# Performance work log

Hardware: AMD Instinct MI355X
Metric: run time of the kernel (lower is better)

The kernel has to match this reference:

```python
import jax, jax.numpy as jnp
import numpy as np

# dims: batch, seq, model dim, heads, head_k_dim, head_v_dim, conv size
B, S, D, H, DK, DV, K = 1, 2048, 1024, 8, 128, 128, 4
KD, VD = H * DK, H * DV  # key_dim, value_dim


def _silu(x):
    return x * jax.nn.sigmoid(x)


def _l2norm(x, eps=1e-6):
    return x * jax.lax.rsqrt(jnp.sum(x * x, -1, keepdims=True) + eps)


def _causal_conv_silu(x, w):
    # depthwise causal conv1d (ShortConvolution, activation='silu', no bias)
    # x: [b, s, d], w: [d, K]
    Kc = w.shape[1]
    xp = jnp.pad(x, ((0, 0), (Kc - 1, 0), (0, 0)))
    y = sum(xp[:, i:i + x.shape[1], :] * w[:, i] for i in range(Kc))
    return _silu(y)


def _rmsnorm(x, w, eps=1e-5):
    return x * jax.lax.rsqrt(jnp.mean(x * x, -1, keepdims=True) + eps) * w


def _kda(q, k, v, g, beta):
    # gated delta-rule linear attention (KDA), recurrent form == chunk_kda math
    # q,k,g: [B,S,H,DK]; v: [B,S,H,DV]; beta: [B,S,H]
    scale = DK ** -0.5
    qn = _l2norm(q) * scale  # use_qk_l2norm_in_kernel=True
    kn = _l2norm(k)

    def step(Sm, inp):
        q_t, k_t, v_t, g_t, b_t = inp  # [B,H,DK], [B,H,DK], [B,H,DV], [B,H,DK], [B,H]
        Sm = Sm * jnp.exp(g_t)[..., None]                    # per-key-channel decay
        v_new = (v_t - jnp.einsum('bhk,bhkv->bhv', k_t, Sm)) * b_t[..., None]
        Sm = Sm + k_t[..., None] * v_new[..., None, :]       # delta-rule update
        o_t = jnp.einsum('bhk,bhkv->bhv', q_t, Sm)
        return Sm, o_t

    xs = (jnp.swapaxes(qn, 0, 1), jnp.swapaxes(kn, 0, 1), jnp.swapaxes(v, 0, 1),
          jnp.swapaxes(g, 0, 1), jnp.swapaxes(beta, 0, 1))
    S0 = jnp.zeros((q.shape[0], H, DK, DV), jnp.float32)
    _, o = jax.lax.scan(step, S0, xs)
    return jnp.swapaxes(o, 0, 1)  # [B,S,H,DV]


def setup_inputs() -> dict:
    key = jax.random.key(0)
    ks = jax.random.split(key, 20)

    def w(k, shape, fan_in):
        return jax.random.normal(k, shape, jnp.float32) / np.sqrt(fan_in)

    return {
        'x': jax.random.normal(ks[0], (B, S, D), jnp.float32),
        've': jax.random.normal(ks[1], (B, S, D), jnp.float32),
        'sa_lambdas': jax.random.uniform(ks[2], (2,), jnp.float32),
        'Wq': w(ks[3], (KD, D), D), 'Wk': w(ks[4], (KD, D), D), 'Wv': w(ks[5], (VD, D), D),
        'Wo': w(ks[6], (D, VD), VD),
        'wq_conv': w(ks[7], (KD, K), K), 'wk_conv': w(ks[8], (KD, K), K), 'wv_conv': w(ks[9], (VD, K), K),
        'Wf1': w(ks[10], (DV, D), D), 'Wf2': w(ks[11], (KD, DV), DV),
        'Wb': w(ks[12], (H, D), D),
        'A_log': jnp.log(jax.random.uniform(ks[13], (H,), jnp.float32, 1.0, 16.0)),
        'dt_bias': jnp.zeros((KD,), jnp.float32),
        'Wg1': w(ks[14], (DV, D), D), 'Wg2': w(ks[15], (VD, DV), DV),
        'bg2': jnp.zeros((VD,), jnp.float32),
        'w_norm': jnp.ones((DV,), jnp.float32),
    }


def reference(x, ve, sa_lambdas, Wq, Wk, Wv, Wo, wq_conv, wk_conv, wv_conv,
              Wf1, Wf2, Wb, A_log, dt_bias, Wg1, Wg2, bg2, w_norm):
    b, s, _ = x.shape
    # q/k/v projections + short causal conv with silu
    q = _causal_conv_silu(x @ Wq.T, wq_conv)
    k = _causal_conv_silu(x @ Wk.T, wk_conv)
    v = _causal_conv_silu(x @ Wv.T, wv_conv)
    # fused_kda_gate: g = -exp(A_log) * softplus(f_proj(x) + dt_bias), per [H, DK]
    g = (x @ Wf1.T) @ Wf2.T
    g = jax.nn.softplus((g + dt_bias).astype(jnp.float32)).reshape(b, s, H, DK)
    g = -jnp.exp(A_log)[None, None, :, None] * g
    beta = jax.nn.sigmoid((x @ Wb.T).astype(jnp.float32))  # [b,s,H]
    q = q.reshape(b, s, H, DK)
    k = k.reshape(b, s, H, DK)
    v = v.reshape(b, s, H, DV)
    # mix v with value-embedding ve (3-D branch of _mix_v_with_ve)
    ve_v = _causal_conv_silu(ve @ Wv.T, wv_conv).reshape(b, s, H, DV)
    v = sa_lambdas[0] * v + sa_lambdas[1] * ve_v
    o = _kda(q, k, v, g, beta)  # [b,s,H,DV]
    # FusedRMSNormGated(activation='sigmoid'): rmsnorm(o)*w then gate
    g_out = ((x @ Wg1.T) @ Wg2.T + bg2).reshape(b, s, H, DV)
    o = _rmsnorm(o, w_norm) * jax.nn.sigmoid(g_out)
    return o.reshape(b, s, VD) @ Wo.T
```

## Files before the change

### kernel.cpp

```cpp
#include <hip/hip_runtime.h>
#include <math.h>
#include <stdint.h>

#define S_LEN 2048
#define DMODEL 1024
#define NH 8
#define DK_ 128
#define DV_ 128
#define KD_ 1024
#define KCONV 4
#define CW 32
#define NW2 64
#define PREB_STRIDE 17408
#define TKH_OFF 0
#define QHT_OFF 4096
#define KCT_OFF 8192
#define TV_OFF 12288
#define NN_OFF 16384
#define RS 164
#define GS 20

typedef short bf16x8 __attribute__((ext_vector_type(8)));
typedef float f32x4 __attribute__((ext_vector_type(4)));

__device__ __forceinline__ uint16_t f2bf(float f) {
  uint32_t u = __float_as_uint(f);
  u += 0x7FFF + ((u >> 16) & 1);
  return (uint16_t)(u >> 16);
}
__device__ __forceinline__ float bf2f(uint16_t u) {
  return __uint_as_float((uint32_t)u << 16);
}
__device__ __forceinline__ void glds16(const uint16_t* g, uint16_t* l) {
  __builtin_amdgcn_global_load_lds(
      (const __attribute__((address_space(1))) void*)g,
      (__attribute__((address_space(3))) void*)l, 16, 0, 0);
}
__device__ __forceinline__ float dot4(float4 a, float4 b) {
  return fmaf(a.w, b.w, fmaf(a.z, b.z, fmaf(a.y, b.y, a.x * b.x)));
}
__device__ __forceinline__ float4 f4add(float4 a, float4 b) {
  float4 r; r.x = a.x + b.x; r.y = a.y + b.y; r.z = a.z + b.z; r.w = a.w + b.w; return r;
}
__device__ __forceinline__ float4 f4sub(float4 a, float4 b) {
  float4 r; r.x = a.x - b.x; r.y = a.y - b.y; r.z = a.z - b.z; r.w = a.w - b.w; return r;
}
__device__ __forceinline__ float4 f4mul(float4 a, float4 b) {
  float4 r; r.x = a.x * b.x; r.y = a.y * b.y; r.z = a.z * b.z; r.w = a.w * b.w; return r;
}
__device__ __forceinline__ float4 f4s(float4 a, float s) {
  float4 r; r.x = a.x * s; r.y = a.y * s; r.z = a.z * s; r.w = a.w * s; return r;
}
__device__ __forceinline__ float4 f4expc(float4 a) {
  float4 r;
  r.x = expf(fminf(a.x, 0.f)); r.y = expf(fminf(a.y, 0.f));
  r.z = expf(fminf(a.z, 0.f)); r.w = expf(fminf(a.w, 0.f));
  return r;
}
__device__ __forceinline__ float4 f4exp(float4 a) {
  float4 r; r.x = expf(a.x); r.y = expf(a.y); r.z = expf(a.z); r.w = expf(a.w); return r;
}
__device__ __forceinline__ uint4 pack8(float4 a, float4 b) {
  uint4 r;
  r.x = (uint32_t)f2bf(a.x) | ((uint32_t)f2bf(a.y) << 16);
  r.y = (uint32_t)f2bf(a.z) | ((uint32_t)f2bf(a.w) << 16);
  r.z = (uint32_t)f2bf(b.x) | ((uint32_t)f2bf(b.y) << 16);
  r.w = (uint32_t)f2bf(b.z) | ((uint32_t)f2bf(b.w) << 16);
  return r;
}
__device__ __forceinline__ uint2 pack4(f32x4 a) {
  uint2 r;
  r.x = (uint32_t)f2bf(a[0]) | ((uint32_t)f2bf(a[1]) << 16);
  r.y = (uint32_t)f2bf(a[2]) | ((uint32_t)f2bf(a[3]) << 16);
  return r;
}
union U4B8 { uint4 u; bf16x8 b; };
__device__ __forceinline__ bf16x8 u2b(uint4 u) { U4B8 x; x.u = u; return x.b; }

#define DPPADD(x, ctrl) \
  x += __int_as_float(__builtin_amdgcn_update_dpp(0, __float_as_int(x), ctrl, 0xF, 0xF, true))

__device__ __forceinline__ void row8_sum2(float& a, float& b) {
  DPPADD(a, 0xB1); DPPADD(b, 0xB1);
  DPPADD(a, 0x4E); DPPADD(b, 0x4E);
  DPPADD(a, 0x141); DPPADD(b, 0x141);
}
__device__ __forceinline__ void row8_arr8x2(float* x, float* y) {
#pragma unroll
  for (int i = 0; i < 8; i++) { DPPADD(x[i], 0xB1); DPPADD(y[i], 0xB1); }
#pragma unroll
  for (int i = 0; i < 8; i++) { DPPADD(x[i], 0x4E); DPPADD(y[i], 0x4E); }
#pragma unroll
  for (int i = 0; i < 8; i++) { DPPADD(x[i], 0x141); DPPADD(y[i], 0x141); }
}

struct CastArgs {
  const float* s[8];
  uint16_t* d[8];
  int n[8];
};
__global__ __launch_bounds__(256) void cast_multi(CastArgs a) {
  int i = blockIdx.y;
  const int step = gridDim.x * 256 * 8;
  for (int base = (blockIdx.x * 256 + threadIdx.x) * 8; base < a.n[i]; base += step) {
    const float4* sp = (const float4*)(a.s[i] + base);
    float4 x0 = sp[0], x1 = sp[1];
    *(uint4*)(a.d[i] + base) = pack8(x0, x1);
  }
}

__global__ __launch_bounds__(256) void gemm_wc(
    const float* __restrict__ A,
    const float* __restrict__ B,
    uint16_t* __restrict__ C) {
  __shared__ float As[16][68];
  __shared__ float Bs[16][68];
  const int tid = threadIdx.x;
  const int m0 = blockIdx.y * 64, n0 = blockIdx.x * 64;
  const int tx = tid & 15, ty = tid >> 4;
  const int lk = tid & 15, lr = tid >> 4;
  const int bc = tid & 63, bkr = tid >> 6;
  float acc[4][4] = {};
  for (int k0 = 0; k0 < 128; k0 += 16) {
#pragma unroll
    for (int i = 0; i < 4; i++) {
      As[lk][lr + 16 * i] = A[(size_t)(m0 + lr + 16 * i) * 128 + k0 + lk];
      Bs[bkr + 4 * i][bc] = B[(size_t)(k0 + bkr + 4 * i) * 1024 + n0 + bc];
    }
    __syncthreads();
#pragma unroll
    for (int kk = 0; kk < 16; kk++) {
      float4 a4 = *(const float4*)&As[kk][ty * 4];
      float4 b4 = *(const float4*)&Bs[kk][tx * 4];
      float av[4] = {a4.x, a4.y, a4.z, a4.w};
      float bv[4] = {b4.x, b4.y, b4.z, b4.w};
#pragma unroll
      for (int i = 0; i < 4; i++)
#pragma unroll
        for (int jx = 0; jx < 4; jx++) acc[i][jx] = fmaf(av[i], bv[jx], acc[i][jx]);
    }
    __syncthreads();
  }
#pragma unroll
  for (int i = 0; i < 4; i++)
#pragma unroll
    for (int jx = 0; jx < 4; jx++)
      C[(size_t)(m0 + ty * 4 + i) * 1024 + n0 + tx * 4 + jx] = f2bf(acc[i][jx]);
}

__global__ __launch_bounds__(256) void pad_wb(const float* __restrict__ Wb,
                                              uint16_t* __restrict__ Wbp) {
  int idx = blockIdx.x * 256 + threadIdx.x;
  if (idx >= 128 * 1024) return;
  int r = idx >> 10;
  Wbp[idx] = (r < 8) ? f2bf(Wb[idx]) : (uint16_t)0;
}

struct GJobs {
  const uint16_t* A[8];
  const uint16_t* B[8];
  void* C[8];
  int N[8];
  int outbf[8];
};
__global__ __launch_bounds__(256) void gemm_mfma(GJobs j, int K) {
  const int z = blockIdx.z;
  const int N = j.N[z];
  const int n0 = blockIdx.x * 128;
  if (n0 >= N) return;
  __shared__ uint16_t Asb[128 * 32];
  __shared__ uint16_t Bsb[128 * 32];
  const uint16_t* __restrict__ A = j.A[z];
  const uint16_t* __restrict__ B = j.B[z];
  const int tid = threadIdx.x;
  const int w = tid >> 6, lane = tid & 63;
  const int m0 = blockIdx.y * 128;
  const int mw = (w & 1) * 64, nw = (w >> 1) * 64;
  const int c0 = tid, c1 = 256 + tid;
  const int r0 = c0 >> 2, cl0 = (c0 & 3) ^ ((r0 >> 2) & 3);
  const int r1 = c1 >> 2, cl1 = (c1 & 3) ^ ((r1 >> 2) & 3);
  const uint16_t* gA0 = A + (size_t)(m0 + r0) * K + cl0 * 8;
  const uint16_t* gA1 = A + (size_t)(m0 + r1) * K + cl1 * 8;
  const uint16_t* gB0 = B + (size_t)(n0 + r0) * K + cl0 * 8;
  const uint16_t* gB1 = B + (size_t)(n0 + r1) * K + cl1 * 8;
  uint16_t* lA0 = Asb + w * 512;
  uint16_t* lA1 = Asb + 2048 + w * 512;
  uint16_t* lB0 = Bsb + w * 512;
  uint16_t* lB1 = Bsb + 2048 + w * 512;

  const int l15 = lane & 15, q = lane >> 4;
  const int ccq = q ^ ((l15 >> 2) & 3);

  f32x4 acc[4][4] = {};
  for (int k0 = 0; k0 < K; k0 += 32) {
    glds16(gA0 + k0, lA0);
    glds16(gA1 + k0, lA1);
    glds16(gB0 + k0, lB0);
    glds16(gB1 + k0, lB1);
    __syncthreads();
    bf16x8 af[4], bfr[4];
#pragma unroll
    for (int i = 0; i < 4; i++)
      af[i] = *(const bf16x8*)&Asb[(mw + i * 16 + l15) * 32 + ccq * 8];
#pragma unroll
    for (int jx = 0; jx < 4; jx++)
      bfr[jx] = *(const bf16x8*)&Bsb[(nw + jx * 16 + l15) * 32 + ccq * 8];
#pragma unroll
    for (int i = 0; i < 4; i++)
#pragma unroll
      for (int jx = 0; jx < 4; jx++)
        acc[i][jx] = __builtin_amdgcn_mfma_f32_16x16x32_bf16(af[i], bfr[jx],
                                                             acc[i][jx], 0, 0, 0);
    __syncthreads();
  }
  const int obf = j.outbf[z];
#pragma unroll
  for (int i = 0; i < 4; i++) {
#pragma unroll
    for (int jx = 0; jx < 4; jx++) {
      int n = n0 + nw + jx * 16 + l15;
#pragma unroll
      for (int r = 0; r < 4; r++) {
        int m = m0 + mw + i * 16 + q * 4 + r;
        if (obf)
          ((uint16_t*)j.C[z])[(size_t)m * N + n] = f2bf(acc[i][jx][r]);
        else
          ((float*)j.C[z])[(size_t)m * N + n] = acc[i][jx][r];
      }
    }
  }
}

__global__ __launch_bounds__(256) void conv_silu_mix(
    const uint16_t* __restrict__ qp, const uint16_t* __restrict__ kp,
    const uint16_t* __restrict__ vp, const uint16_t* __restrict__ vep,
    const float* __restrict__ wq, const float* __restrict__ wk,
    const float* __restrict__ wv, const float* __restrict__ lam,
    float* __restrict__ qc, float* __restrict__ kc, float* __restrict__ vmx) {
  int idx = blockIdx.x * 256 + threadIdx.x;
  if (idx >= S_LEN * KD_) return;
  int s = idx >> 10, d = idx & 1023;
  float aq = 0.f, ak = 0.f, av = 0.f, ae = 0.f;
#pragma unroll
  for (int i = 0; i < KCONV; i++) {
    int ss = s - (KCONV - 1) + i;
    if (ss < 0) continue;
    size_t off = (size_t)ss * KD_ + d;
    aq = fmaf(bf2f(qp[off]), wq[d * KCONV + i], aq);
    ak = fmaf(bf2f(kp[off]), wk[d * KCONV + i], ak);
    av = fmaf(bf2f(vp[off]), wv[d * KCONV + i], av);
    ae = fmaf(bf2f(vep[off]), wv[d * KCONV + i], ae);
  }
  qc[idx] = aq / (1.f + expf(-aq));
  kc[idx] = ak / (1.f + expf(-ak));
  float sv = av / (1.f + expf(-av));
  float se = ae / (1.f + expf(-ae));
  vmx[idx] = lam[0] * sv + lam[1] * se;
}

__global__ __launch_bounds__(256) void kda_pre(
    const float* __restrict__ qc, const float* __restrict__ kc,
    const float* __restrict__ graw, const float* __restrict__ vm,
    const float* __restrict__ bpre, const float* __restrict__ dt_bias,
    const float* __restrict__ A_log, uint16_t* __restrict__ preB,
    float* __restrict__ preF) {
  __shared__ float kls[32 * RS];
  __shared__ float Gls[32 * RS];
  __shared__ float khls[32 * 132];
  __shared__ float Mcm[32 * 36];
  __shared__ float bls[32];
  const int w = blockIdx.x >> 3, h = blockIdx.x & 7;
  const int tid = threadIdx.x;
  const int t = tid >> 3, kq = tid & 7;
  const int wv = tid >> 6;
  const size_t gb = (size_t)blockIdx.x * PREB_STRIDE;
  const size_t gf = (size_t)blockIdx.x * 128;

  size_t roff = (size_t)(w * CW + t) * KD_ + h * DK_ + kq * 16;
  float4 kv[4], qv[4], gv[4], dtb[4];
#pragma unroll
  for (int i = 0; i < 4; i++) {
    kv[i] = *(const float4*)(kc + roff + i * 4);
    qv[i] = *(const float4*)(qc + roff + i * 4);
    gv[i] = *(const float4*)(graw + roff + i * 4);
    dtb[i] = *(const float4*)(dt_bias + h * DK_ + kq * 16 + i * 4);
  }
  const float Ahead = expf(A_log[h]);
  if (tid < 32) {
    float b = bpre[(size_t)(w * CW + tid) * 128 + h];
    bls[tid] = 1.f / (1.f + expf(-b));
  }
  float src[32];
  if (tid >= 128) {
    int c2 = tid - 128;
#pragma unroll
    for (int t2 = 0; t2 < 32; t2++)
      src[t2] = vm[(size_t)(w * CW + t2) * KD_ + h * DV_ + c2];
  }
#pragma unroll
  for (int i = 0; i < 4; i++) {
    float vsp[4];
    float xin[4] = {gv[i].x + dtb[i].x, gv[i].y + dtb[i].y,
                    gv[i].z + dtb[i].z, gv[i].w + dtb[i].w};
#pragma unroll
    for (int e = 0; e < 4; e++)
      vsp[e] = (xin[e] > 20.f) ? xin[e] : log1pf(expf(xin[e]));
    gv[i].x = -Ahead * vsp[0]; gv[i].y = -Ahead * vsp[1];
    gv[i].z = -Ahead * vsp[2]; gv[i].w = -Ahead * vsp[3];
  }
  float sk = 0.f, sq = 0.f;
#pragma unroll
  for (int i = 0; i < 4; i++) {
    sk += dot4(kv[i], kv[i]);
    sq += dot4(qv[i], qv[i]);
  }
  row8_sum2(sk, sq);
  float rkn = rsqrtf(sk + 1e-6f);
  float rqn = rsqrtf(sq + 1e-6f) * 0.08838834764831845f;
#pragma unroll
  for (int i = 0; i < 4; i++) {
    kv[i] = f4s(kv[i], rkn);
    qv[i] = f4s(qv[i], rqn);
    *(float4*)&kls[t * RS + kq * GS + i * 4] = kv[i];
    *(float4*)&Gls[t * RS + kq * GS + i * 4] = gv[i];
  }
  __syncthreads();
  float4 Ga[4] = {};
#pragma unroll
  for (int jb = 0; jb < 4; jb++) {
    if (jb <= wv) {
#pragma unroll
      for (int jj = 0; jj < 8; jj++) {
        int j = jb * 8 + jj;
        bool inc = (jb < wv) || (j <= t);
#pragma unroll
        for (int i = 0; i < 4; i++) {
          float4 gj = *(const float4*)&Gls[j * RS + kq * GS + i * 4];
          if (inc) Ga[i] = f4add(Ga[i], gj);
        }
      }
    }
  }
  __syncthreads();
  float4 Pa[4];
#pragma unroll
  for (int i = 0; i < 4; i++) {
    *(float4*)&Gls[t * RS + kq * GS + i * 4] = Ga[i];
    Pa[i] = f4exp(Ga[i]);
    float4 kh = f4mul(kv[i], Pa[i]);
    *(float4*)&khls[t * 132 + kq * 16 + i * 4] = kh;
  }
  {
    float4 q0 = f4mul(qv[0], Pa[0]), q1 = f4mul(qv[1], Pa[1]);
    float4 q2 = f4mul(qv[2], Pa[2]), q3 = f4mul(qv[3], Pa[3]);
    *(uint4*)(preB + gb + QHT_OFF + t * 128 + kq * 16) = pack8(q0, q1);
    *(uint4*)(preB + gb + QHT_OFF + t * 128 + kq * 16 + 8) = pack8(q2, q3);
  }
  if (t == 31) {
#pragma unroll
    for (int i = 0; i < 4; i++)
      *(float4*)(preF + gf + kq * 16 + i * 4) = Pa[i];
  }
  __syncthreads();
#pragma unroll
  for (int i = 0; i < 4; i++) {
    float4 Gfi = *(const float4*)&Gls[31 * RS + kq * GS + i * 4];
    float4 ea = f4expc(f4sub(Gfi, Ga[i]));
    float4 kc4 = f4mul(kv[i], ea);
    float kk[4] = {kc4.x, kc4.y, kc4.z, kc4.w};
#pragma unroll
    for (int e = 0; e < 4; e++)
      preB[gb + KCT_OFF + (kq * 16 + i * 4 + e) * 32 + t] = f2bf(kk[e]);
  }
#pragma unroll
  for (int jb = 0; jb < 4; jb++) {
    if (jb <= wv) {
      float mp8[8], np8[8];
#pragma unroll
      for (int jj = 0; jj < 8; jj++) {
        int j = jb * 8 + jj;
        float m = 0.f, n = 0.f;
#pragma unroll
        for (int i = 0; i < 4; i++) {
          float4 kj = *(const float4*)&kls[j * RS + kq * GS + i * 4];
          float4 Gj = *(const float4*)&Gls[j * RS + kq * GS + i * 4];
          float4 e = f4expc(f4sub(Ga[i], Gj));
          float4 p = f4mul(kj, e);
          m += dot4(kv[i], p);
          n += dot4(qv[i], p);
        }
        mp8[jj] = (j < t) ? m : 0.f;
        np8[jj] = (j <= t) ? n : 0.f;
      }
      row8_arr8x2(mp8, np8);
#pragma unroll
      for (int jj = 0; jj < 8; jj++) {
        if (kq == jj) {
          int j = jb * 8 + jj;
          Mcm[j * 36 + t] = bls[t] * mp8[jj];
          preB[gb + NN_OFF + t * 32 + j] = f2bf(np8[jj]);
        }
      }
    } else {
      preB[gb + NN_OFF + t * 32 + jb * 8 + kq] = 0;
    }
  }
  float bl[32];
#pragma unroll
  for (int i = 0; i < 8; i++) {
    float4 b4 = *(const float4*)&bls[i * 4];
    bl[i * 4 + 0] = b4.x; bl[i * 4 + 1] = b4.y;
    bl[i * 4 + 2] = b4.z; bl[i * 4 + 3] = b4.w;
  }
  if (tid < 128) {
#pragma unroll
    for (int t2 = 0; t2 < 32; t2++) src[t2] = khls[t2 * 132 + tid];
  }
  __syncthreads();
  const int c = tid;
  float acc[32];
#pragma unroll
  for (int i = 0; i < 32; i++) acc[i] = 0.f;
#pragma unroll
  for (int t2 = 0; t2 < 32; t2++) {
    float val = fmaf(bl[t2], src[t2], -acc[t2]);
    if (c < 128)
      preB[gb + TKH_OFF + t2 * 128 + c] = f2bf(val);
    else
      preB[gb + TV_OFF + t2 * 128 + (c - 128)] = f2bf(val);
#pragma unroll
    for (int t3 = t2 + 1; t3 < 32; t3++)
      acc[t3] = fmaf(Mcm[t2 * 36 + t3], val, acc[t3]);
  }
}

__global__ __launch_bounds__(128) void kda_scan(
    const uint16_t* __restrict__ preB, const float* __restrict__ preF,
    float* __restrict__ o) {
  __shared__ uint16_t tkh[2][32 * 136];
  __shared__ uint16_t qht[2][32 * 136];
  __shared__ uint16_t sbf[16 * 136];
  __shared__ uint16_t vbf[16 * 40];
  const int h = blockIdx.x & 7, cg = blockIdx.x >> 3;
  const int tid = threadIdx.x;
  const int wv = tid >> 6, lane = tid & 63;
  const int q = lane >> 4, l15 = lane & 15;

  auto stage = [&](int w, int buf) {
    size_t gbs = (size_t)(w * 8 + h) * PREB_STRIDE;
    const uint4* gt = (const uint4*)(preB + gbs + TKH_OFF);
    const uint4* gq = (const uint4*)(preB + gbs + QHT_OFF);
    int row = lane >> 1, half = lane & 1;
    uint4 a[8], b[8];
#pragma unroll
    for (int i = 0; i < 8; i++) {
      a[i] = gt[lane * 8 + i];
      b[i] = gq[lane * 8 + i];
    }
#pragma unroll
    for (int i = 0; i < 8; i++) {
      *(uint4*)&tkh[buf][row * 136 + half * 64 + i * 8] = a[i];
      *(uint4*)&qht[buf][row * 136 + half * 64 + i * 8] = b[i];
    }
  };

  f32x4 s[8] = {};

  if (wv == 1) stage(0, 0);
  __syncthreads();

  for (int w = 0; w < NW2; w++) {
    if (wv == 1) {
      if (w + 1 < NW2) stage(w + 1, (w + 1) & 1);
    } else {
      const int buf = w & 1;
      const size_t gbs = (size_t)(w * 8 + h) * PREB_STRIDE;
      uint4 kct[8], nrg[2];
      float4 pb[8];
      float tvv[2][4];
#pragma unroll
      for (int ki = 0; ki < 8; ki++)
        kct[ki] = *(const uint4*)(preB + gbs + KCT_OFF + (16 * ki + l15) * 32 + q * 8);
#pragma unroll
      for (int tt = 0; tt < 2; tt++)
        nrg[tt] = *(const uint4*)(preB + gbs + NN_OFF + (tt * 16 + l15) * 32 + q * 8);
#pragma unroll
      for (int ki = 0; ki < 8; ki++)
        pb[ki] = *(const float4*)(preF + (size_t)(w * 8 + h) * 128 + 16 * ki + q * 4);
#pragma unroll
      for (int tt = 0; tt < 2; tt++)
#pragma unroll
        for (int r = 0; r < 4; r++)
          tvv[tt][r] = bf2f(preB[gbs + TV_OFF + (tt * 16 + q * 4 + r) * 128 + cg * 16 + l15]);
#pragma unroll
      for (int ki = 0; ki < 8; ki++)
        *(uint2*)&sbf[l15 * 136 + 16 * ki + q * 4] = pack4(s[ki]);
      f32x4 aat[2] = {}, bbt[2] = {};
#pragma unroll
      for (int kc = 0; kc < 4; kc++) {
        bf16x8 bS = *(const bf16x8*)&sbf[l15 * 136 + kc * 32 + q * 8];
#pragma unroll
        for (int tt = 0; tt < 2; tt++) {
          bf16x8 aT = *(const bf16x8*)&tkh[buf][(tt * 16 + l15) * 136 + kc * 32 + q * 8];
          bf16x8 aQ = *(const bf16x8*)&qht[buf][(tt * 16 + l15) * 136 + kc * 32 + q * 8];
          aat[tt] = __builtin_amdgcn_mfma_f32_16x16x32_bf16(aT, bS, aat[tt], 0, 0, 0);
          bbt[tt] = __builtin_amdgcn_mfma_f32_16x16x32_bf16(aQ, bS, bbt[tt], 0, 0, 0);
        }
      }
#pragma unroll
      for (int tt = 0; tt < 2; tt++) {
        f32x4 vn;
#pragma unroll
        for (int r = 0; r < 4; r++) vn[r] = tvv[tt][r] - aat[tt][r];
        *(uint2*)&vbf[l15 * 40 + tt * 16 + q * 4] = pack4(vn);
      }
      bf16x8 bV = *(const bf16x8*)&vbf[l15 * 40 + q * 8];
#pragma unroll
      for (int tt = 0; tt < 2; tt++) {
        f32x4 ot = __builtin_amdgcn_mfma_f32_16x16x32_bf16(u2b(nrg[tt]), bV,
                                                           bbt[tt], 0, 0, 0);
#pragma unroll
        for (int r = 0; r < 4; r++)
          o[(size_t)(w * CW + tt * 16 + q * 4 + r) * KD_ + h * DK_ + cg * 16 + l15] = ot[r];
      }
#pragma unroll
      for (int ki = 0; ki < 8; ki++) {
#pragma unroll
        for (int r = 0; r < 4; r++) s[ki][r] *= pb[ki][r];
        s[ki] = __builtin_amdgcn_mfma_f32_16x16x32_bf16(u2b(kct[ki]), bV, s[ki], 0, 0, 0);
      }
    }
    __syncthreads();
  }
}

__global__ __launch_bounds__(64) void gated_rmsnorm(
    const float* __restrict__ o, const float* __restrict__ g2raw,
    const float* __restrict__ bg2, const float* __restrict__ wn,
    uint16_t* __restrict__ ob) {
  size_t base = (size_t)blockIdx.x * DV_;
  int t = threadIdx.x;
  float a = o[base + t], b = o[base + t + 64];
  float ss = a * a + b * b;
#pragma unroll
  for (int off = 32; off > 0; off >>= 1) ss += __shfl_xor(ss, off);
  float r = rsqrtf(ss * (1.f / 128.f) + 1e-5f);
  int c0 = (int)((base + t) & 1023), c1 = (int)((base + t + 64) & 1023);
  float ga = 1.f / (1.f + expf(-(g2raw[base + t] + bg2[c0])));
  float gb = 1.f / (1.f + expf(-(g2raw[base + t + 64] + bg2[c1])));
  ob[base + t] = f2bf(a * r * wn[t] * ga);
  ob[base + t + 64] = f2bf(b * r * wn[t + 64] * gb);
}

extern "C" void kernel_launch(void* const* d_in, const int* in_sizes, int n_in,
                              void* d_out, int out_size, void* d_ws, size_t ws_size,
                              hipStream_t stream) {
  const float* x = (const float*)d_in[0];
  const float* ve = (const float*)d_in[1];
  const float* lam = (const float*)d_in[2];
  const float* Wq = (const float*)d_in[3];
  const float* Wk = (const float*)d_in[4];
  const float* Wv = (const float*)d_in[5];
  const float* Wo = (const float*)d_in[6];
  const float* wq_conv = (const float*)d_in[7];
  const float* wk_conv = (const float*)d_in[8];
  const float* wv_conv = (const float*)d_in[9];
  const float* Wf1 = (const float*)d_in[10];
  const float* Wf2 = (const float*)d_in[11];
  const float* Wb = (const float*)d_in[12];
  const float* A_log = (const float*)d_in[13];
  const float* dt_bias = (const float*)d_in[14];
  const float* Wg1 = (const float*)d_in[15];
  const float* Wg2 = (const float*)d_in[16];
  const float* bg2 = (const float*)d_in[17];
  const float* w_norm = (const float*)d_in[18];
  float* out = (float*)d_out;

  float* ws = (float*)d_ws;
  const size_t SZ = (size_t)S_LEN * KD_;
  uint16_t* qpb = (uint16_t*)ws;
  uint16_t* kpb = (uint16_t*)(ws + SZ / 2);
  uint16_t* vpb = (uint16_t*)(ws + SZ);
  uint16_t* vepb = (uint16_t*)(ws + 3 * SZ / 2);
  float* q_c = ws + 2 * SZ;
  float* k_c = ws + 3 * SZ;
  float* v_mix = ws + 4 * SZ;
  float* graw = ws + 5 * SZ;
  float* o_buf = graw;
  float* g2raw = k_c;
  uint16_t* bws = (uint16_t*)(ws + 6 * SZ);
  uint16_t* xb = bws;
  uint16_t* veb = xb + SZ;
  uint16_t* Wqb = veb + SZ;
  uint16_t* Wkb = Wqb + (size_t)KD_ * DMODEL;
  uint16_t* Wvb = Wkb + (size_t)KD_ * DMODEL;
  uint16_t* Wob = Wvb + (size_t)KD_ * DMODEL;
  uint16_t* Wg1b = Wob + (size_t)DMODEL * KD_;
  uint16_t* Wg2b = Wg1b + (size_t)DV_ * DMODEL;
  uint16_t* Wcb = Wg2b + (size_t)KD_ * DV_;
  uint16_t* Wbp = Wcb + (size_t)KD_ * DMODEL;
  uint16_t* g1b = Wbp + (size_t)128 * 1024;
  uint16_t* ob = g1b + (size_t)S_LEN * DV_;
  float* bpre2 = ws + 18 * (size_t)1024 * 1024;
  float* preF = ws + (size_t)20 * 1024 * 1024;
  uint16_t* preB = (uint16_t*)(ws + (size_t)20 * 1024 * 1024 + 65536 + 64);

  dim3 blk(256);
  int ew_blocks = (S_LEN * KD_ + 255) / 256;

  CastArgs ca;
  ca.s[0] = x;   ca.d[0] = xb;   ca.n[0] = S_LEN * DMODEL;
  ca.s[1] = ve;  ca.d[1] = veb;  ca.n[1] = S_LEN * DMODEL;
  ca.s[2] = Wq;  ca.d[2] = Wqb;  ca.n[2] = KD_ * DMODEL;
  ca.s[3] = Wk;  ca.d[3] = Wkb;  ca.n[3] = KD_ * DMODEL;
  ca.s[4] = Wv;  ca.d[4] = Wvb;  ca.n[4] = KD_ * DMODEL;
  ca.s[5] = Wo;  ca.d[5] = Wob;  ca.n[5] = DMODEL * KD_;
  ca.s[6] = Wg1; ca.d[6] = Wg1b; ca.n[6] = DV_ * DMODEL;
  ca.s[7] = Wg2; ca.d[7] = Wg2b; ca.n[7] = KD_ * DV_;
  cast_multi<<<dim3(256, 8), blk, 0, stream>>>(ca);

  gemm_wc<<<dim3(16, 16), blk, 0, stream>>>(Wf2, Wf1, Wcb);
  pad_wb<<<dim3(512), blk, 0, stream>>>(Wb, Wbp);

  GJobs jq;
  jq.A[0] = xb;  jq.B[0] = Wqb;  jq.C[0] = qpb;   jq.N[0] = KD_; jq.outbf[0] = 1;
  jq.A[1] = xb;  jq.B[1] = Wkb;  jq.C[1] = kpb;   jq.N[1] = KD_; jq.outbf[1] = 1;
  jq.A[2] = xb;  jq.B[2] = Wvb;  jq.C[2] = vpb;   jq.N[2] = KD_; jq.outbf[2] = 1;
  jq.A[3] = veb; jq.B[3] = Wvb;  jq.C[3] = vepb;  jq.N[3] = KD_; jq.outbf[3] = 1;
  jq.A[4] = xb;  jq.B[4] = Wg1b; jq.C[4] = g1b;   jq.N[4] = DV_; jq.outbf[4] = 1;
  jq.A[5] = xb;  jq.B[5] = Wcb;  jq.C[5] = graw;  jq.N[5] = KD_; jq.outbf[5] = 0;
  jq.A[6] = xb;  jq.B[6] = Wbp;  jq.C[6] = bpre2; jq.N[6] = 128; jq.outbf[6] = 0;
  gemm_mfma<<<dim3(8, 16, 7), blk, 0, stream>>>(jq, DMODEL);

  conv_silu_mix<<<ew_blocks, blk, 0, stream>>>(qpb, kpb, vpb, vepb,
                                               wq_conv, wk_conv, wv_conv, lam,
                                               q_c, k_c, v_mix);

  kda_pre<<<dim3(NW2 * 8), blk, 0, stream>>>(q_c, k_c, graw, v_mix, bpre2,
                                             dt_bias, A_log, preB, preF);
  kda_scan<<<dim3(64), dim3(128), 0, stream>>>(preB, preF, o_buf);

  GJobs jg2;
  jg2.A[0] = g1b; jg2.B[0] = Wg2b; jg2.C[0] = g2raw; jg2.N[0] = KD_; jg2.outbf[0] = 0;
  gemm_mfma<<<dim3(8, 16, 1), blk, 0, stream>>>(jg2, DV_);

  gated_rmsnorm<<<dim3(S_LEN * NH), dim3(64), 0, stream>>>(o_buf, g2raw, bg2,
                                                           w_norm, ob);

  GJobs jo;
  jo.A[0] = ob; jo.B[0] = Wob; jo.C[0] = out; jo.N[0] = DMODEL; jo.outbf[0] = 0;
  gemm_mfma<<<dim3(8, 16, 1), blk, 0, stream>>>(jo, KD_);
}
```

Measured before the change: 389.3 us.

## Software-pipeline scan window loads with register double-buffering in both waves

Restructures the kda_scan loop so the staging wave keeps two windows of tkh/qht data in flight in registers before writing them to shared memory. The compute wave also prefetches its per-window operands (kct, nrg, decay, tv) one iteration ahead in two register sets, hiding global-load latency behind the serial MFMA recurrence. Both waves run separate loops that must match barrier counts. This raises register pressure and adds redundant clamped reloads on the last iterations.

```diff
diff --git a/kernel.cpp b/kernel.cpp
--- a/kernel.cpp
+++ b/kernel.cpp
@@ -446,38 +446,43 @@
   const int wv = tid >> 6, lane = tid & 63;
   const int q = lane >> 4, l15 = lane & 15;
 
-  auto stage = [&](int w, int buf) {
-    size_t gbs = (size_t)(w * 8 + h) * PREB_STRIDE;
-    const uint4* gt = (const uint4*)(preB + gbs + TKH_OFF);
-    const uint4* gq = (const uint4*)(preB + gbs + QHT_OFF);
-    int row = lane >> 1, half = lane & 1;
-    uint4 a[8], b[8];
-#pragma unroll
-    for (int i = 0; i < 8; i++) {
-      a[i] = gt[lane * 8 + i];
-      b[i] = gq[lane * 8 + i];
+  if (wv == 1) {
+    const int row = lane >> 1, half = lane & 1;
+    auto sload = [&](uint4 (&a)[8], uint4 (&b)[8], int w) {
+      size_t gbs = (size_t)(w * 8 + h) * PREB_STRIDE;
+      const uint4* gt = (const uint4*)(preB + gbs + TKH_OFF);
+      const uint4* gq = (const uint4*)(preB + gbs + QHT_OFF);
+#pragma unroll
+      for (int i = 0; i < 8; i++) {
+        a[i] = gt[lane * 8 + i];
+        b[i] = gq[lane * 8 + i];
+      }
+    };
+    auto swrite = [&](uint4 (&a)[8], uint4 (&b)[8], int buf) {
+#pragma unroll
+      for (int i = 0; i < 8; i++) {
+        *(uint4*)&tkh[buf][row * 136 + half * 64 + i * 8] = a[i];
+        *(uint4*)&qht[buf][row * 136 + half * 64 + i * 8] = b[i];
+      }
+    };
+    uint4 aA[8], bA[8], aB[8], bB[8];
+    sload(aA, bA, 0);
+    sload(aB, bB, 1);
+    swrite(aA, bA, 0);
+    __syncthreads();
+    for (int w = 0; w < NW2; w += 2) {
+      if (w + 2 < NW2) sload(aA, bA, w + 2);
+      swrite(aB, bB, 1);
+      __syncthreads();
+      if (w + 3 < NW2) sload(aB, bB, w + 3);
+      if (w + 2 < NW2) swrite(aA, bA, 0);
+      __syncthreads();
     }
-#pragma unroll
-    for (int i = 0; i < 8; i++) {
-      *(uint4*)&tkh[buf][row * 136 + half * 64 + i * 8] = a[i];
-      *(uint4*)&qht[buf][row * 136 + half * 64 + i * 8] = b[i];
-    }
-  };
-
-  f32x4 s[8] = {};
-
-  if (wv == 1) stage(0, 0);
-  __syncthreads();
-
-  for (int w = 0; w < NW2; w++) {
-    if (wv == 1) {
-      if (w + 1 < NW2) stage(w + 1, (w + 1) & 1);
-    } else {
-      const int buf = w & 1;
-      const size_t gbs = (size_t)(w * 8 + h) * PREB_STRIDE;
-      uint4 kct[8], nrg[2];
-      float4 pb[8];
-      float tvv[2][4];
+  } else {
+    f32x4 s[8] = {};
+    auto pload = [&](uint4 (&kct)[8], uint4 (&nrg)[2], float4 (&pb)[8],
+                     uint16_t (&tv)[8], int w) {
+      size_t gbs = (size_t)(w * 8 + h) * PREB_STRIDE;
 #pragma unroll
       for (int ki = 0; ki < 8; ki++)
         kct[ki] = *(const uint4*)(preB + gbs + KCT_OFF + (16 * ki + l15) * 32 + q * 8);
@@ -491,7 +496,11 @@
       for (int tt = 0; tt < 2; tt++)
 #pragma unroll
         for (int r = 0; r < 4; r++)
-          tvv[tt][r] = bf2f(preB[gbs + TV_OFF + (tt * 16 + q * 4 + r) * 128 + cg * 16 + l15]);
+          tv[tt * 4 + r] =
+              preB[gbs + TV_OFF + (tt * 16 + q * 4 + r) * 128 + cg * 16 + l15];
+    };
+    auto compute = [&](uint4 (&kct)[8], uint4 (&nrg)[2], float4 (&pb)[8],
+                       uint16_t (&tv)[8], int buf, int w) {
 #pragma unroll
       for (int ki = 0; ki < 8; ki++)
         *(uint2*)&sbf[l15 * 136 + 16 * ki + q * 4] = pack4(s[ki]);
@@ -511,7 +520,7 @@
       for (int tt = 0; tt < 2; tt++) {
         f32x4 vn;
 #pragma unroll
-        for (int r = 0; r < 4; r++) vn[r] = tvv[tt][r] - aat[tt][r];
+        for (int r = 0; r < 4; r++) vn[r] = bf2f(tv[tt * 4 + r]) - aat[tt][r];
         *(uint2*)&vbf[l15 * 40 + tt * 16 + q * 4] = pack4(vn);
       }
       bf16x8 bV = *(const bf16x8*)&vbf[l15 * 40 + q * 8];
@@ -521,7 +530,8 @@
                                                            bbt[tt], 0, 0, 0);
 #pragma unroll
         for (int r = 0; r < 4; r++)
-          o[(size_t)(w * CW + tt * 16 + q * 4 + r) * KD_ + h * DK_ + cg * 16 + l15] = ot[r];
+          o[(size_t)(w * CW + tt * 16 + q * 4 + r) * KD_ + h * DK_ + cg * 16 + l15] =
+              ot[r];
       }
 #pragma unroll
       for (int ki = 0; ki < 8; ki++) {
@@ -529,8 +539,20 @@
         for (int r = 0; r < 4; r++) s[ki][r] *= pb[ki][r];
         s[ki] = __builtin_amdgcn_mfma_f32_16x16x32_bf16(u2b(kct[ki]), bV, s[ki], 0, 0, 0);
       }
+    };
+    uint4 kA[8], nA[2]; float4 pA[8]; uint16_t tA[8];
+    uint4 kB[8], nB[2]; float4 pB[8]; uint16_t tB[8];
+    pload(kA, nA, pA, tA, 0);
+    pload(kB, nB, pB, tB, 1);
+    __syncthreads();
+    for (int w = 0; w < NW2; w += 2) {
+      compute(kA, nA, pA, tA, 0, w);
+      pload(kA, nA, pA, tA, (w + 2 < NW2) ? w + 2 : w);
+      __syncthreads();
+      compute(kB, nB, pB, tB, 1, w + 1);
+      pload(kB, nB, pB, tB, (w + 3 < NW2) ? w + 3 : w + 1);
+      __syncthreads();
     }
-    __syncthreads();
   }
 }
 
```

Result: slower. 605.9 us (+55.6%).
